# Performance work log

Hardware: AMD Instinct MI355X
Metric: run time of the kernel (lower is better)

## Reference

```python
import jax, jax.numpy as jnp
import numpy as np

IN_CH = 256
OUT_CH = 128
N = 6144
ADJ_P = 0.01  # edge density -> avg degree ~61


def setup_inputs() -> dict:
    key = jax.random.key(0)
    ks = jax.random.split(key, 8)
    x = jax.random.normal(ks[0], (1, IN_CH, N), dtype=jnp.float32)
    adj = (jax.random.uniform(ks[1], (N, N)) < ADJ_P).astype(jnp.float32)
    W_fts = jax.random.normal(ks[2], (OUT_CH, IN_CH), dtype=jnp.float32) * 0.05
    w1 = jax.random.normal(ks[3], (OUT_CH,), dtype=jnp.float32) * 0.05
    b1 = jnp.zeros((1,), dtype=jnp.float32)
    w2 = jax.random.normal(ks[4], (OUT_CH,), dtype=jnp.float32) * 0.05
    b2 = jnp.zeros((1,), dtype=jnp.float32)
    vars_bias = jax.random.normal(ks[5], (1, N, OUT_CH), dtype=jnp.float32) * 0.02
    return {"x": x, "adj": adj, "W_fts": W_fts, "w1": w1, "b1": b1,
            "w2": w2, "b2": b2, "vars_bias": vars_bias}


def reference(x, adj, W_fts, w1, b1, w2, b2, vars_bias):
    # fts = Conv1d(in, out, k=1, bias=False)(x): [1, OUT_CH, N]
    fts = jnp.einsum('oi,bin->bon', W_fts, x)
    f = fts[0]  # [OUT_CH, N]
    # f1/f2 = Conv1d(out, 1, 1)(fts) -> per-node scalars [N]
    f1 = jnp.einsum('o,on->n', w1, f) + b1  # [N]
    f2 = jnp.einsum('o,on->n', w2, f) + b2  # [N]
    # scores[i,j] = leaky_relu(adj[i,j]*f1[i] + adj[i,j]*f2[j], 0.2)
    scores = jax.nn.leaky_relu(adj * f1[:, None] + adj * f2[None, :], 0.2)
    # sparse_softmax2d: per-row softmax masked to nonzero entries
    mask = (scores != 0).astype(scores.dtype)
    m = jnp.max(scores, axis=1, keepdims=True)  # stabilizer; cancels in ratio
    exps = jnp.exp(scores - m) * mask
    coefs = exps / jnp.sum(exps, axis=1, keepdims=True)  # [N, N]
    # vals = coefs @ fts.T : [N, OUT_CH]
    vals = coefs @ f.T
    # add bias, permute to [1, OUT_CH, N]
    ret = jnp.transpose(vals[None, :, :] + vars_bias, (0, 2, 1))
    return ret
```

## Files before the change

kernel.cpp:

```cpp
#include <hip/hip_runtime.h>

#define NN  6144
#define ICH 256
#define OCH 128
#define QW  160

typedef float vf4 __attribute__((ext_vector_type(4)));

__global__ __launch_bounds__(256) void k_fts(const float* __restrict__ x,
        const float* __restrict__ W, const float* __restrict__ w1,
        const float* __restrict__ w2, float* __restrict__ ft,
        float* __restrict__ f1, float* __restrict__ f2) {
    __shared__ float xs[32][32];
    __shared__ float Ws[32][OCH + 4];
    const int n0  = blockIdx.x * 32;
    const int tid = threadIdx.x;
    const int oq = (tid & 31) * 4;
    const int nq = (tid >> 5) * 4;
    float acc[4][4] = {};
    for (int k0 = 0; k0 < ICH; k0 += 32) {
        __syncthreads();
        {
            const int nn = tid & 31;
            const int kb = tid >> 5;
#pragma unroll
            for (int r = 0; r < 4; ++r)
                xs[kb + r * 8][nn] = x[(size_t)(k0 + kb + r * 8) * NN + n0 + nn];
        }
        {
            const int kk = tid & 31;
            const int ob = tid >> 5;
#pragma unroll
            for (int r = 0; r < 16; ++r) {
                const int o = ob + r * 8;
                Ws[kk][o] = W[o * ICH + k0 + kk];
            }
        }
        __syncthreads();
#pragma unroll
        for (int kk = 0; kk < 32; ++kk) {
            const float4 xv = *(const float4*)&xs[kk][nq];
            const float4 wv = *(const float4*)&Ws[kk][oq];
            const float xa[4] = {xv.x, xv.y, xv.z, xv.w};
            const float wa[4] = {wv.x, wv.y, wv.z, wv.w};
#pragma unroll
            for (int a = 0; a < 4; ++a)
#pragma unroll
                for (int b = 0; b < 4; ++b)
                    acc[a][b] = fmaf(xa[a], wa[b], acc[a][b]);
        }
    }
#pragma unroll
    for (int a = 0; a < 4; ++a) {
        float4 v = make_float4(acc[a][0], acc[a][1], acc[a][2], acc[a][3]);
        *(float4*)&ft[(size_t)(n0 + nq + a) * OCH + oq] = v;
    }
    const float4 w1v = *(const float4*)(w1 + oq);
    const float4 w2v = *(const float4*)(w2 + oq);
    float p1[4], p2[4];
#pragma unroll
    for (int a = 0; a < 4; ++a) {
        p1[a] = acc[a][0] * w1v.x + acc[a][1] * w1v.y + acc[a][2] * w1v.z + acc[a][3] * w1v.w;
        p2[a] = acc[a][0] * w2v.x + acc[a][1] * w2v.y + acc[a][2] * w2v.z + acc[a][3] * w2v.w;
    }
#pragma unroll
    for (int m = 16; m > 0; m >>= 1) {
#pragma unroll
        for (int a = 0; a < 4; ++a) {
            p1[a] += __shfl_xor(p1[a], m);
            p2[a] += __shfl_xor(p2[a], m);
        }
    }
    if ((tid & 31) == 0) {
#pragma unroll
        for (int a = 0; a < 4; ++a) {
            f1[n0 + nq + a] = p1[a];
            f2[n0 + nq + a] = p2[a];
        }
    }
}

__global__ __launch_bounds__(256) void k_attn(const float* __restrict__ adj,
        const float* __restrict__ ft, const float* __restrict__ f1,
        const float* __restrict__ f2, const float* __restrict__ b1,
        const float* __restrict__ b2, const float* __restrict__ vb,
        float* __restrict__ vals) {
    __shared__ int   qw[4][QW];
    __shared__ int   eq_j[4][QW];
    __shared__ float eq_e[4][QW];
    __shared__ int   qc[4];
    const int tid  = threadIdx.x;
    const int lane = tid & 63;
    const int wave = tid >> 6;
    const int i = (blockIdx.x & 7) * 768 + (blockIdx.x >> 3) * 4 + wave;
    if (lane == 0) qc[wave] = 0;
    const float s1 = f1[i] + b1[0] + b2[0];
    const float* arow = adj + (size_t)i * NN;
    vf4 ab[2][6];
#pragma unroll
    for (int w = 0; w < 6; ++w)
        ab[0][w] = __builtin_nontemporal_load((const vf4*)(arow + lane * 4 + w * 256));
#pragma unroll
    for (int b = 0; b < 4; ++b) {
        if (b < 3) {
#pragma unroll
            for (int w = 0; w < 6; ++w)
                ab[(b + 1) & 1][w] = __builtin_nontemporal_load(
                    (const vf4*)(arow + (b + 1) * 1536 + lane * 4 + w * 256));
        }
#pragma unroll
        for (int w = 0; w < 6; ++w) {
            const vf4 a4 = ab[b & 1][w];
            const int j0 = b * 1536 + w * 256 + lane * 4;
            const int m = (a4.x != 0.f ? 1 : 0) | (a4.y != 0.f ? 2 : 0)
                        | (a4.z != 0.f ? 4 : 0) | (a4.w != 0.f ? 8 : 0);
            if (m) {
                const int slot = atomicAdd(&qc[wave], 1);
                if (slot < QW) qw[wave][slot] = (j0 << 4) | m;
            }
        }
    }
    const int nW = qc[wave] < QW ? qc[wave] : QW;
    float den = 0.f;
    int off0 = 0;
    for (int t0 = 0; t0 < nW; t0 += 64) {
        const int t = t0 + lane;
        int jb = 0, mm = 0, kc = 0;
        float e0 = 0.f, e1 = 0.f, e2 = 0.f, e3 = 0.f;
        if (t < nW) {
            const int entry = qw[wave][t];
            jb = entry >> 4; mm = entry & 15;
            kc = __popc(mm);
            const float4 g = *(const float4*)(f2 + jb);
            if (mm & 1) { float s = s1 + g.x; s = s > 0.f ? s : 0.2f * s; e0 = __expf(s); den += e0; }
            if (mm & 2) { float s = s1 + g.y; s = s > 0.f ? s : 0.2f * s; e1 = __expf(s); den += e1; }
            if (mm & 4) { float s = s1 + g.z; s = s > 0.f ? s : 0.2f * s; e2 = __expf(s); den += e2; }
            if (mm & 8) { float s = s1 + g.w; s = s > 0.f ? s : 0.2f * s; e3 = __expf(s); den += e3; }
        }
        int pf = kc;
#pragma unroll
        for (int off = 1; off < 64; off <<= 1) {
            const int y = __shfl_up(pf, off);
            if (lane >= off) pf += y;
        }
        int slot = off0 + pf - kc;
        off0 += __shfl(pf, 63);
        if (t < nW) {
            if (mm & 1) { if (slot < QW) { eq_j[wave][slot] = jb;     eq_e[wave][slot] = e0; } ++slot; }
            if (mm & 2) { if (slot < QW) { eq_j[wave][slot] = jb + 1; eq_e[wave][slot] = e1; } ++slot; }
            if (mm & 4) { if (slot < QW) { eq_j[wave][slot] = jb + 2; eq_e[wave][slot] = e2; } ++slot; }
            if (mm & 8) { if (slot < QW) { eq_j[wave][slot] = jb + 3; eq_e[wave][slot] = e3; } ++slot; }
        }
    }
#pragma unroll
    for (int off = 32; off > 0; off >>= 1) den += __shfl_xor(den, off);
    const float inv = 1.f / den;
    const int nE = off0 < QW ? off0 : QW;
    const int half = lane >> 5;
    const int c0 = (lane & 31) * 4;
    float4 nm = make_float4(0.f, 0.f, 0.f, 0.f);
#pragma unroll 4
    for (int idx = half; idx < nE; idx += 2) {
        const int   j = eq_j[wave][idx];
        const float e = eq_e[wave][idx];
        const float4 g = *(const float4*)(ft + (size_t)j * OCH + c0);
        nm.x = fmaf(e, g.x, nm.x);
        nm.y = fmaf(e, g.y, nm.y);
        nm.z = fmaf(e, g.z, nm.z);
        nm.w = fmaf(e, g.w, nm.w);
    }
    nm.x += __shfl_xor(nm.x, 32);
    nm.y += __shfl_xor(nm.y, 32);
    nm.z += __shfl_xor(nm.z, 32);
    nm.w += __shfl_xor(nm.w, 32);
    if (half == 0) {
        const float4 bv = *(const float4*)(vb + (size_t)i * OCH + c0);
        float4 r;
        r.x = fmaf(nm.x, inv, bv.x);
        r.y = fmaf(nm.y, inv, bv.y);
        r.z = fmaf(nm.z, inv, bv.z);
        r.w = fmaf(nm.w, inv, bv.w);
        *(float4*)&vals[(size_t)i * OCH + c0] = r;
    }
}

__global__ __launch_bounds__(256) void k_tr(const float* __restrict__ v,
                                            float* __restrict__ out) {
    __shared__ float t[32][33];
    const int i0 = blockIdx.x * 32;
    const int c0 = blockIdx.y * 32;
    const int r = threadIdx.x >> 3;
    const int q = (threadIdx.x & 7) * 4;
    const float4 a = *(const float4*)&v[(size_t)(i0 + r) * OCH + c0 + q];
    t[r][q] = a.x; t[r][q + 1] = a.y; t[r][q + 2] = a.z; t[r][q + 3] = a.w;
    __syncthreads();
    const float4 o = make_float4(t[q][r], t[q + 1][r], t[q + 2][r], t[q + 3][r]);
    *(float4*)&out[(size_t)(c0 + r) * NN + i0 + q] = o;
}

extern "C" void kernel_launch(void* const* d_in, const int* in_sizes, int n_in,
                              void* d_out, int out_size, void* d_ws, size_t ws_size,
                              hipStream_t stream) {
    const float* x   = (const float*)d_in[0];
    const float* adj = (const float*)d_in[1];
    const float* W   = (const float*)d_in[2];
    const float* w1  = (const float*)d_in[3];
    const float* b1  = (const float*)d_in[4];
    const float* w2  = (const float*)d_in[5];
    const float* b2  = (const float*)d_in[6];
    const float* vb  = (const float*)d_in[7];
    float* out = (float*)d_out;

    char* ws = (char*)d_ws;
    float* ft   = (float*)ws;
    float* f1   = (float*)(ws + 3145728);
    float* f2   = (float*)(ws + 3145728 + 24576);
    float* vals = (float*)(ws + 3145728 + 49152);

    k_fts<<<dim3(NN / 32), 256, 0, stream>>>(x, W, w1, w2, ft, f1, f2);
    k_attn<<<dim3(NN / 4), 256, 0, stream>>>(adj, ft, f1, f2, b1, b2, vb, vals);
    k_tr<<<dim3(NN / 32, OCH / 32), 256, 0, stream>>>(vals, out);
}
```

Baseline: 256.2 us.

## Pack adjacency into bitmask in a separate kernel before attention

A new kernel streams the dense adjacency matrix with wide, fully coalesced loads and packs it into a 16-bit-per-16-column bitmask. The attention kernel then reads compact 32-bit mask words per row and compacts edges with a popcount prefix scan instead of shared-memory atomics. The intent is to decouple the bandwidth-bound adjacency scan from the per-row gather/compute and to remove atomic contention. It adds an extra kernel launch and a mask write/read round trip, and the per-lane ctz loop can be imbalanced across lanes.

```diff
diff --git a/kernel.cpp b/kernel.cpp
--- a/kernel.cpp
+++ b/kernel.cpp
@@ -80,82 +80,77 @@
     }
 }
 
-__global__ __launch_bounds__(256) void k_attn(const float* __restrict__ adj,
+__global__ __launch_bounds__(256) void k_pack(const float* __restrict__ adj,
+        unsigned short* __restrict__ msk) {
+    const int tid = threadIdx.x;
+    const size_t base = (size_t)blockIdx.x * 24576;
+#pragma unroll
+    for (int t = 0; t < 6; ++t) {
+        const size_t f0 = base + (size_t)t * 4096 + (size_t)tid * 16;
+        const vf4 v0 = __builtin_nontemporal_load((const vf4*)(adj + f0));
+        const vf4 v1 = __builtin_nontemporal_load((const vf4*)(adj + f0 + 4));
+        const vf4 v2 = __builtin_nontemporal_load((const vf4*)(adj + f0 + 8));
+        const vf4 v3 = __builtin_nontemporal_load((const vf4*)(adj + f0 + 12));
+        unsigned int m = 0;
+        m |= (v0.x != 0.f ? 1u : 0u) << 0;  m |= (v0.y != 0.f ? 1u : 0u) << 1;
+        m |= (v0.z != 0.f ? 1u : 0u) << 2;  m |= (v0.w != 0.f ? 1u : 0u) << 3;
+        m |= (v1.x != 0.f ? 1u : 0u) << 4;  m |= (v1.y != 0.f ? 1u : 0u) << 5;
+        m |= (v1.z != 0.f ? 1u : 0u) << 6;  m |= (v1.w != 0.f ? 1u : 0u) << 7;
+        m |= (v2.x != 0.f ? 1u : 0u) << 8;  m |= (v2.y != 0.f ? 1u : 0u) << 9;
+        m |= (v2.z != 0.f ? 1u : 0u) << 10; m |= (v2.w != 0.f ? 1u : 0u) << 11;
+        m |= (v3.x != 0.f ? 1u : 0u) << 12; m |= (v3.y != 0.f ? 1u : 0u) << 13;
+        m |= (v3.z != 0.f ? 1u : 0u) << 14; m |= (v3.w != 0.f ? 1u : 0u) << 15;
+        msk[f0 >> 4] = (unsigned short)m;
+    }
+}
+
+__global__ __launch_bounds__(256) void k_attn2(const unsigned int* __restrict__ msk,
         const float* __restrict__ ft, const float* __restrict__ f1,
         const float* __restrict__ f2, const float* __restrict__ b1,
         const float* __restrict__ b2, const float* __restrict__ vb,
         float* __restrict__ vals) {
-    __shared__ int   qw[4][QW];
     __shared__ int   eq_j[4][QW];
     __shared__ float eq_e[4][QW];
-    __shared__ int   qc[4];
     const int tid  = threadIdx.x;
     const int lane = tid & 63;
     const int wave = tid >> 6;
     const int i = (blockIdx.x & 7) * 768 + (blockIdx.x >> 3) * 4 + wave;
-    if (lane == 0) qc[wave] = 0;
     const float s1 = f1[i] + b1[0] + b2[0];
-    const float* arow = adj + (size_t)i * NN;
-    vf4 ab[2][6];
-#pragma unroll
-    for (int w = 0; w < 6; ++w)
-        ab[0][w] = __builtin_nontemporal_load((const vf4*)(arow + lane * 4 + w * 256));
-#pragma unroll
-    for (int b = 0; b < 4; ++b) {
-        if (b < 3) {
-#pragma unroll
-            for (int w = 0; w < 6; ++w)
-                ab[(b + 1) & 1][w] = __builtin_nontemporal_load(
-                    (const vf4*)(arow + (b + 1) * 1536 + lane * 4 + w * 256));
-        }
-#pragma unroll
-        for (int w = 0; w < 6; ++w) {
-            const vf4 a4 = ab[b & 1][w];
-            const int j0 = b * 1536 + w * 256 + lane * 4;
-            const int m = (a4.x != 0.f ? 1 : 0) | (a4.y != 0.f ? 2 : 0)
-                        | (a4.z != 0.f ? 4 : 0) | (a4.w != 0.f ? 8 : 0);
-            if (m) {
-                const int slot = atomicAdd(&qc[wave], 1);
-                if (slot < QW) qw[wave][slot] = (j0 << 4) | m;
-            }
-        }
-    }
-    const int nW = qc[wave] < QW ? qc[wave] : QW;
+    const unsigned int* mrow = msk + (size_t)i * 192;
+    unsigned int w[3];
+    w[0] = mrow[lane];
+    w[1] = mrow[lane + 64];
+    w[2] = mrow[lane + 128];
+    const int kc = __popc(w[0]) + __popc(w[1]) + __popc(w[2]);
+    int pf = kc;
+#pragma unroll
+    for (int off = 1; off < 64; off <<= 1) {
+        const int y = __shfl_up(pf, off);
+        if (lane >= off) pf += y;
+    }
+    const int nT = __shfl(pf, 63);
+    int slot = pf - kc;
     float den = 0.f;
-    int off0 = 0;
-    for (int t0 = 0; t0 < nW; t0 += 64) {
-        const int t = t0 + lane;
-        int jb = 0, mm = 0, kc = 0;
-        float e0 = 0.f, e1 = 0.f, e2 = 0.f, e3 = 0.f;
-        if (t < nW) {
-            const int entry = qw[wave][t];
-            jb = entry >> 4; mm = entry & 15;
-            kc = __popc(mm);
-            const float4 g = *(const float4*)(f2 + jb);
-            if (mm & 1) { float s = s1 + g.x; s = s > 0.f ? s : 0.2f * s; e0 = __expf(s); den += e0; }
-            if (mm & 2) { float s = s1 + g.y; s = s > 0.f ? s : 0.2f * s; e1 = __expf(s); den += e1; }
-            if (mm & 4) { float s = s1 + g.z; s = s > 0.f ? s : 0.2f * s; e2 = __expf(s); den += e2; }
-            if (mm & 8) { float s = s1 + g.w; s = s > 0.f ? s : 0.2f * s; e3 = __expf(s); den += e3; }
-        }
-        int pf = kc;
-#pragma unroll
-        for (int off = 1; off < 64; off <<= 1) {
-            const int y = __shfl_up(pf, off);
-            if (lane >= off) pf += y;
-        }
-        int slot = off0 + pf - kc;
-        off0 += __shfl(pf, 63);
-        if (t < nW) {
-            if (mm & 1) { if (slot < QW) { eq_j[wave][slot] = jb;     eq_e[wave][slot] = e0; } ++slot; }
-            if (mm & 2) { if (slot < QW) { eq_j[wave][slot] = jb + 1; eq_e[wave][slot] = e1; } ++slot; }
-            if (mm & 4) { if (slot < QW) { eq_j[wave][slot] = jb + 2; eq_e[wave][slot] = e2; } ++slot; }
-            if (mm & 8) { if (slot < QW) { eq_j[wave][slot] = jb + 3; eq_e[wave][slot] = e3; } ++slot; }
+#pragma unroll
+    for (int s = 0; s < 3; ++s) {
+        unsigned int ww = w[s];
+        const int jbase = (lane + s * 64) * 32;
+        while (ww) {
+            const int b = __builtin_ctz(ww);
+            ww &= ww - 1;
+            const int j = jbase + b;
+            float sc = s1 + f2[j];
+            sc = sc > 0.f ? sc : 0.2f * sc;
+            const float e = __expf(sc);
+            den += e;
+            if (slot < QW) { eq_j[wave][slot] = j; eq_e[wave][slot] = e; }
+            ++slot;
         }
     }
 #pragma unroll
     for (int off = 32; off > 0; off >>= 1) den += __shfl_xor(den, off);
     const float inv = 1.f / den;
-    const int nE = off0 < QW ? off0 : QW;
+    const int nE = nT < QW ? nT : QW;
     const int half = lane >> 5;
     const int c0 = (lane & 31) * 4;
     float4 nm = make_float4(0.f, 0.f, 0.f, 0.f);
@@ -215,9 +210,12 @@
     float* ft   = (float*)ws;
     float* f1   = (float*)(ws + 3145728);
     float* f2   = (float*)(ws + 3145728 + 24576);
-    float* vals = (float*)(ws + 3145728 + 49152);
+    float* vals = (float*)(ws + 3194880);
+    void*  msk  = (void*)(ws + 3194880 + 3145728);
 
     k_fts<<<dim3(NN / 32), 256, 0, stream>>>(x, W, w1, w2, ft, f1, f2);
-    k_attn<<<dim3(NN / 4), 256, 0, stream>>>(adj, ft, f1, f2, b1, b2, vb, vals);
+    k_pack<<<dim3(1536), 256, 0, stream>>>(adj, (unsigned short*)msk);
+    k_attn2<<<dim3(NN / 4), 256, 0, stream>>>((const unsigned int*)msk, ft, f1, f2,
+                                              b1, b2, vb, vals);
     k_tr<<<dim3(NN / 32, OCH / 32), 256, 0, stream>>>(vals, out);
 }
```

Measured after the change: 279.3 us. 1.09x slower.
